# Kernel optimization log

Measured on AMD Instinct MI355X. Metric: run time of the kernel, lower is better.

Reference implementation:

```python
import jax, jax.numpy as jnp
import numpy as np

B, T, C, H = 2, 2048, 1024, 16  # batch, seq, d_model, heads
D = C // H                       # head dim = 64


def setup_inputs() -> dict:
    key = jax.random.key(0)
    ks = jax.random.split(key, 5)
    s = 0.02  # init scale for weights
    return {
        "x": jax.random.normal(ks[0], (B, T, C), jnp.float32),
        "Wq": jax.random.normal(ks[1], (C, C), jnp.float32) * s,
        "bq": jnp.zeros((C,), jnp.float32),
        "Wk": jax.random.normal(ks[2], (C, C), jnp.float32) * s,
        "bk": jnp.zeros((C,), jnp.float32),
        "Wv": jax.random.normal(ks[3], (C, C), jnp.float32) * s,
        "bv": jnp.zeros((C,), jnp.float32),
        "Wo": jax.random.normal(ks[4], (C, C), jnp.float32) * s,
        "bo": jnp.zeros((C,), jnp.float32),
    }


def reference(x, Wq, bq, Wk, bk, Wv, bv, Wo, bo):
    b, t, c = x.shape
    h, d = H, C // H
    # QKV projections (torch Linear: x @ W.T + b), split into heads: b h t d
    q = (x @ Wq.T + bq).reshape(b, t, h, d).transpose(0, 2, 1, 3)
    k = (x @ Wk.T + bk).reshape(b, t, h, d).transpose(0, 2, 1, 3)
    v = (x @ Wv.T + bv).reshape(b, t, h, d).transpose(0, 2, 1, 3)

    scale = 1.0 / float(np.sqrt(d))
    att = jnp.einsum("bhqd,bhkd->bhqk", q, k) * scale  # [B,H,T,T]
    causal = jnp.tril(jnp.ones((t, t), dtype=bool))
    att = jnp.where(causal[None, None, :, :], att, -jnp.inf)
    att = jax.nn.softmax(att, axis=-1)
    att_weights = att  # attn_dropout with p=0 is identity

    y = jnp.einsum("bhqk,bhkd->bhqd", att, v)          # [B,H,T,D]
    y = y.transpose(0, 2, 1, 3).reshape(b, t, c)        # b q (h d)
    y = y @ Wo.T + bo                                   # out proj; resid_dropout p=0
    return y, att_weights
```

## Files before the change

kernel.cpp:

```cpp
#include <hip/hip_runtime.h>

#define DI __device__ __forceinline__

typedef __attribute__((ext_vector_type(8))) short short8;
typedef __attribute__((ext_vector_type(4))) float floatx4;
typedef unsigned short u16;

#define Bb 2
#define Tt 2048
#define Cc 1024
#define Hh 16
#define Dd 64
#define C1 0.1803368801111244f
#define NEGBIG (-1e30f)

DI float bf2f(u16 u) { union { unsigned int i; float f; } v; v.i = ((unsigned int)u) << 16; return v.f; }
DI u16 f2bf(float f) {
  union { float f; unsigned int i; } v; v.f = f;
  unsigned int i = v.i;
  unsigned int r = i + 0x7fffu + ((i >> 16) & 1u);
  return (u16)(r >> 16);
}

DI floatx4 mfma16(short8 a, short8 b, floatx4 c) {
  return __builtin_amdgcn_mfma_f32_16x16x32_bf16(a, b, c, 0, 0, 0);
}

DI void gload16(const u16* g, u16* l) {
  __builtin_amdgcn_global_load_lds(
      (const __attribute__((address_space(1))) unsigned int*)(g),
      (__attribute__((address_space(3))) unsigned int*)(l), 16, 0, 0);
}

DI uint4 load8(const void* p, size_t eoff, int isbf) {
  if (isbf) {
    return *(const uint4*)((const u16*)p + eoff);
  } else {
    const float* f = (const float*)p + eoff;
    float4 a = *(const float4*)f;
    float4 b = *(const float4*)(f + 4);
    union { uint4 u; u16 s[8]; } r;
    r.s[0] = f2bf(a.x); r.s[1] = f2bf(a.y); r.s[2] = f2bf(a.z); r.s[3] = f2bf(a.w);
    r.s[4] = f2bf(b.x); r.s[5] = f2bf(b.y); r.s[6] = f2bf(b.z); r.s[7] = f2bf(b.w);
    return r.u;
  }
}

DI float loadb(const void* p, int i, int isbf) {
  return isbf ? bf2f(((const u16*)p)[i]) : ((const float*)p)[i];
}

__global__ void detect_dtype(const u16* __restrict__ x, int* __restrict__ flag) {
  __shared__ int cnt[256];
  int c = 0;
  for (int i = threadIdx.x; i < 4096; i += 256) {
    unsigned u = x[2 * i];
    unsigned e = (u >> 7) & 0xFFu;
    c += (e == 0u || (e >= 100u && e <= 150u)) ? 1 : 0;
  }
  cnt[threadIdx.x] = c;
  __syncthreads();
  for (int s = 128; s > 0; s >>= 1) {
    if ((int)threadIdx.x < s) cnt[threadIdx.x] += cnt[threadIdx.x + s];
    __syncthreads();
  }
  if (threadIdx.x == 0) *flag = (cnt[0] > 2458) ? 1 : 0;
}

__global__ __launch_bounds__(256) void convert_all(
    const void* __restrict__ x,
    const void* __restrict__ wq, const void* __restrict__ wk,
    const void* __restrict__ wv, const void* __restrict__ wo,
    u16* __restrict__ xb,
    u16* __restrict__ wqb, u16* __restrict__ wkb,
    u16* __restrict__ wvb, u16* __restrict__ wob,
    const int* __restrict__ flagp) {
  const int isbf = *flagp;
  const void* src;
  u16* dst;
  size_t n;
  switch (blockIdx.y) {
    case 0: src = x;  dst = xb;  n = (size_t)Bb * Tt * Cc; break;
    case 1: src = wq; dst = wqb; n = (size_t)Cc * Cc; break;
    case 2: src = wk; dst = wkb; n = (size_t)Cc * Cc; break;
    case 3: src = wv; dst = wvb; n = (size_t)Cc * Cc; break;
    default: src = wo; dst = wob; n = (size_t)Cc * Cc; break;
  }
  size_t i8 = ((size_t)blockIdx.x * 256 + threadIdx.x) * 8;
  size_t step = (size_t)gridDim.x * 256 * 8;
  for (; i8 < n; i8 += step) {
    uint4 v = load8(src, i8, isbf);
    *(uint4*)(dst + i8) = v;
  }
}

__global__ __launch_bounds__(256) void qkv_gemm(
    const u16* __restrict__ Xb,
    const u16* __restrict__ Wqb, const u16* __restrict__ Wkb, const u16* __restrict__ Wvb,
    const void* __restrict__ bq, const void* __restrict__ bk, const void* __restrict__ bv,
    u16* __restrict__ Qb, u16* __restrict__ Kb, u16* __restrict__ Vb,
    const int* __restrict__ flagp) {
  __shared__ __align__(16) u16 As[128 * 32];
  __shared__ __align__(16) u16 Bs[128 * 32];
  const int isbf = *flagp;
  const int z = blockIdx.z;
  const u16* W = (z == 0) ? Wqb : (z == 1) ? Wkb : Wvb;
  const void* bias = (z == 0) ? bq : (z == 1) ? bk : bv;
  u16* Out = (z == 0) ? Qb : (z == 1) ? Kb : Vb;

  const int m0 = blockIdx.y * 128, n0 = blockIdx.x * 128;
  const int tid = threadIdx.x;
  const int w = tid >> 6, lane = tid & 63, quad = lane >> 4, l15 = lane & 15;
  const int wm = w >> 1, wn = w & 1;

  floatx4 acc[4][4];
#pragma unroll
  for (int a = 0; a < 4; ++a)
#pragma unroll
    for (int b2 = 0; b2 < 4; ++b2) acc[a][b2] = (floatx4){0.f, 0.f, 0.f, 0.f};

  const int s0 = w * 128 + lane, s1 = s0 + 64;
  const int rA0 = s0 >> 2, c0 = (s0 & 3) * 8;
  const int rA1 = s1 >> 2, c1 = (s1 & 3) * 8;
  const u16* gA0 = Xb + (size_t)(m0 + rA0) * Cc + c0;
  const u16* gA1 = Xb + (size_t)(m0 + rA1) * Cc + c1;
  const u16* gB0 = W + (size_t)(n0 + rA0) * Cc + c0;
  const u16* gB1 = W + (size_t)(n0 + rA1) * Cc + c1;
  u16* lA0 = As + w * 1024;
  u16* lA1 = As + w * 1024 + 512;
  u16* lB0 = Bs + w * 1024;
  u16* lB1 = Bs + w * 1024 + 512;

  for (int k0 = 0; k0 < Cc; k0 += 32) {
    __syncthreads();
    gload16(gA0 + k0, lA0);
    gload16(gA1 + k0, lA1);
    gload16(gB0 + k0, lB0);
    gload16(gB1 + k0, lB1);
    __syncthreads();
    short8 af[4], bfv[4];
#pragma unroll
    for (int t = 0; t < 4; ++t)
      af[t] = *(const short8*)(As + (wm * 64 + t * 16 + l15) * 32 + quad * 8);
#pragma unroll
    for (int t = 0; t < 4; ++t)
      bfv[t] = *(const short8*)(Bs + (wn * 64 + t * 16 + l15) * 32 + quad * 8);
#pragma unroll
    for (int tm = 0; tm < 4; ++tm)
#pragma unroll
      for (int tn = 0; tn < 4; ++tn) acc[tm][tn] = mfma16(af[tm], bfv[tn], acc[tm][tn]);
  }

  float bb[4];
#pragma unroll
  for (int tn = 0; tn < 4; ++tn) bb[tn] = loadb(bias, n0 + wn * 64 + tn * 16 + l15, isbf);
#pragma unroll
  for (int tm = 0; tm < 4; ++tm) {
#pragma unroll
    for (int tn = 0; tn < 4; ++tn) {
      int n = n0 + wn * 64 + tn * 16 + l15;
      int h = n >> 6, d = n & 63;
#pragma unroll
      for (int r = 0; r < 4; ++r) {
        int m = m0 + wm * 64 + tm * 16 + quad * 4 + r;
        int b = m >> 11, t = m & 2047;
        Out[(((size_t)(b * Hh + h) * Tt) + t) * Dd + d] = f2bf(acc[tm][tn][r] + bb[tn]);
      }
    }
  }
}

__global__ __launch_bounds__(256) void out_gemm(
    const u16* __restrict__ Y, const u16* __restrict__ Wob, const void* __restrict__ bo,
    float* __restrict__ Out, const int* __restrict__ flagp) {
  __shared__ __align__(16) u16 As[128 * 32];
  __shared__ __align__(16) u16 Bs[128 * 32];
  const int isbf = *flagp;
  const int m0 = blockIdx.y * 128, n0 = blockIdx.x * 128;
  const int tid = threadIdx.x;
  const int w = tid >> 6, lane = tid & 63, quad = lane >> 4, l15 = lane & 15;
  const int wm = w >> 1, wn = w & 1;

  floatx4 acc[4][4];
#pragma unroll
  for (int a = 0; a < 4; ++a)
#pragma unroll
    for (int b2 = 0; b2 < 4; ++b2) acc[a][b2] = (floatx4){0.f, 0.f, 0.f, 0.f};

  const int s0 = w * 128 + lane, s1 = s0 + 64;
  const int rA0 = s0 >> 2, c0 = (s0 & 3) * 8;
  const int rA1 = s1 >> 2, c1 = (s1 & 3) * 8;
  const u16* gA0 = Y + (size_t)(m0 + rA0) * Cc + c0;
  const u16* gA1 = Y + (size_t)(m0 + rA1) * Cc + c1;
  const u16* gB0 = Wob + (size_t)(n0 + rA0) * Cc + c0;
  const u16* gB1 = Wob + (size_t)(n0 + rA1) * Cc + c1;
  u16* lA0 = As + w * 1024;
  u16* lA1 = As + w * 1024 + 512;
  u16* lB0 = Bs + w * 1024;
  u16* lB1 = Bs + w * 1024 + 512;

  for (int k0 = 0; k0 < Cc; k0 += 32) {
    __syncthreads();
    gload16(gA0 + k0, lA0);
    gload16(gA1 + k0, lA1);
    gload16(gB0 + k0, lB0);
    gload16(gB1 + k0, lB1);
    __syncthreads();
    short8 af[4], bfv[4];
#pragma unroll
    for (int t = 0; t < 4; ++t)
      af[t] = *(const short8*)(As + (wm * 64 + t * 16 + l15) * 32 + quad * 8);
#pragma unroll
    for (int t = 0; t < 4; ++t)
      bfv[t] = *(const short8*)(Bs + (wn * 64 + t * 16 + l15) * 32 + quad * 8);
#pragma unroll
    for (int tm = 0; tm < 4; ++tm)
#pragma unroll
      for (int tn = 0; tn < 4; ++tn) acc[tm][tn] = mfma16(af[tm], bfv[tn], acc[tm][tn]);
  }

  float bb[4];
#pragma unroll
  for (int tn = 0; tn < 4; ++tn) bb[tn] = loadb(bo, n0 + wn * 64 + tn * 16 + l15, isbf);
#pragma unroll
  for (int tm = 0; tm < 4; ++tm)
#pragma unroll
    for (int tn = 0; tn < 4; ++tn) {
      int n = n0 + wn * 64 + tn * 16 + l15;
#pragma unroll
      for (int r = 0; r < 4; ++r) {
        int m = m0 + wm * 64 + tm * 16 + quad * 4 + r;
        Out[(size_t)m * Cc + n] = acc[tm][tn][r] + bb[tn];
      }
    }
}

__global__ __launch_bounds__(256) void attn_kernel(
    const u16* __restrict__ Qbuf, const u16* __restrict__ Kbuf, const u16* __restrict__ Vbuf,
    float* __restrict__ Att, u16* __restrict__ Ybuf) {
  __shared__ __align__(16) u16 Qs[16 * 72];
  __shared__ __align__(16) u16 Ks[128 * 72];
  __shared__ __align__(16) u16 Vts[64 * 136];
  __shared__ __align__(16) u16 Ps[16 * 136];
  __shared__ float redM[4][16], redL[4][16];
  __shared__ float Mfin[16], Lfin[16];

  const int qt = blockIdx.x, h = blockIdx.y, b = blockIdx.z;
  const int q0 = qt * 16, q_hi = q0 + 15;
  const int tid = threadIdx.x;
  const int w = tid >> 6, lane = tid & 63, quad = lane >> 4, l15 = lane & 15;

  const size_t headoff = (size_t)(b * Hh + h) * Tt * Dd;
  const u16* Qh = Qbuf + headoff;
  const u16* Kh = Kbuf + headoff;
  const u16* Vh = Vbuf + headoff;
  float* attO = Att + (size_t)(b * Hh + h) * Tt * Tt;

  {
    int row = tid >> 4, c4 = tid & 15;
    *(uint2*)(Qs + row * 72 + c4 * 4) = *(const uint2*)(Qh + (size_t)(q0 + row) * Dd + c4 * 4);
  }
  __syncthreads();
  short8 aq0 = *(const short8*)(Qs + l15 * 72 + quad * 8);
  short8 aq1 = *(const short8*)(Qs + l15 * 72 + 32 + quad * 8);

  float m4[4], l4[4];
#pragma unroll
  for (int r = 0; r < 4; ++r) { m4[r] = NEGBIG; l4[r] = 0.f; }

  const int nact = (q_hi + 1 + 127) / 128;

  for (int c = 0; c < nact; ++c) {
    const int kb = c * 128;
    __syncthreads();
#pragma unroll
    for (int i = 0; i < 4; ++i) {
      int slot = tid + i * 256;
      int row = slot >> 3, c8 = slot & 7;
      *(uint4*)(Ks + row * 72 + c8 * 8) = *(const uint4*)(Kh + (size_t)(kb + row) * Dd + c8 * 8);
    }
    __syncthreads();
#pragma unroll
    for (int tile = 0; tile < 2; ++tile) {
      int kloc = w * 32 + tile * 16;
      floatx4 acc = (floatx4){0.f, 0.f, 0.f, 0.f};
      short8 b0 = *(const short8*)(Ks + (kloc + l15) * 72 + quad * 8);
      short8 b1 = *(const short8*)(Ks + (kloc + l15) * 72 + 32 + quad * 8);
      acc = mfma16(aq0, b0, acc);
      acc = mfma16(aq1, b1, acc);
      int key = kb + kloc + l15;
#pragma unroll
      for (int r = 0; r < 4; ++r) {
        int qi = q0 + quad * 4 + r;
        if (key <= qi) {
          float s2 = acc[r] * C1;
          float mo = m4[r];
          float mn = fmaxf(mo, s2);
          l4[r] = l4[r] * exp2f(mo - mn) + exp2f(s2 - mn);
          m4[r] = mn;
        }
      }
    }
  }

#pragma unroll
  for (int r = 0; r < 4; ++r) {
    float m = m4[r], l = l4[r];
#pragma unroll
    for (int off = 8; off >= 1; off >>= 1) {
      float mo = __shfl_xor(m, off, 64);
      float lo = __shfl_xor(l, off, 64);
      float mn = fmaxf(m, mo);
      l = l * exp2f(m - mn) + lo * exp2f(mo - mn);
      m = mn;
    }
    m4[r] = m; l4[r] = l;
  }
  if (l15 == 0) {
#pragma unroll
    for (int r = 0; r < 4; ++r) { redM[w][quad * 4 + r] = m4[r]; redL[w][quad * 4 + r] = l4[r]; }
  }
  __syncthreads();
  if (tid < 16) {
    float m = NEGBIG;
#pragma unroll
    for (int w2 = 0; w2 < 4; ++w2) m = fmaxf(m, redM[w2][tid]);
    float l = 0.f;
#pragma unroll
    for (int w2 = 0; w2 < 4; ++w2) l += redL[w2][tid] * exp2f(redM[w2][tid] - m);
    Mfin[tid] = m;
    Lfin[tid] = 1.0f / l;
  }
  __syncthreads();

  floatx4 yacc = (floatx4){0.f, 0.f, 0.f, 0.f};

  for (int c = 0; c < Tt / 128; ++c) {
    const int kb = c * 128;
    if (kb > q_hi) {
      uint4 z; z.x = 0u; z.y = 0u; z.z = 0u; z.w = 0u;
#pragma unroll
      for (int i = 0; i < 2; ++i) {
        int slot = tid + i * 256;
        int row = slot >> 5, g = slot & 31;
        *(uint4*)(attO + (size_t)(q0 + row) * Tt + kb + g * 4) = z;
      }
      continue;
    }
    __syncthreads();
#pragma unroll
    for (int i = 0; i < 4; ++i) {
      int slot = tid + i * 256;
      int row = slot >> 3, c8 = slot & 7;
      *(uint4*)(Ks + row * 72 + c8 * 8) = *(const uint4*)(Kh + (size_t)(kb + row) * Dd + c8 * 8);
    }
    {
      int row = tid >> 1, cb = (tid & 1) * 32;
      const u16* src = Vh + (size_t)(kb + row) * Dd + cb;
      union { uint4 u; u16 s[8]; } cv;
#pragma unroll
      for (int g = 0; g < 4; ++g) {
        cv.u = *(const uint4*)(src + g * 8);
#pragma unroll
        for (int j = 0; j < 8; ++j) Vts[(cb + g * 8 + j) * 136 + row] = cv.s[j];
      }
    }
    __syncthreads();

#pragma unroll
    for (int tile = 0; tile < 2; ++tile) {
      int kloc = w * 32 + tile * 16;
      floatx4 acc = (floatx4){0.f, 0.f, 0.f, 0.f};
      short8 b0 = *(const short8*)(Ks + (kloc + l15) * 72 + quad * 8);
      short8 b1 = *(const short8*)(Ks + (kloc + l15) * 72 + 32 + quad * 8);
      acc = mfma16(aq0, b0, acc);
      acc = mfma16(aq1, b1, acc);
      int key = kb + kloc + l15;
#pragma unroll
      for (int r = 0; r < 4; ++r) {
        int row = quad * 4 + r;
        int qi = q0 + row;
        float p = 0.f;
        if (key <= qi) p = exp2f(fminf(acc[r] * C1 - Mfin[row], 0.f)) * Lfin[row];
        attO[(size_t)qi * Tt + key] = p;
        Ps[row * 136 + kloc + l15] = f2bf(p);
      }
    }
    __syncthreads();

#pragma unroll
    for (int ks = 0; ks < 4; ++ks) {
      short8 ap = *(const short8*)(Ps + l15 * 136 + ks * 32 + quad * 8);
      short8 bv = *(const short8*)(Vts + (w * 16 + l15) * 136 + ks * 32 + quad * 8);
      yacc = mfma16(ap, bv, yacc);
    }
  }

#pragma unroll
  for (int r = 0; r < 4; ++r) {
    int qi = q0 + quad * 4 + r;
    Ybuf[(size_t)(b * Tt + qi) * Cc + h * Dd + w * 16 + l15] = f2bf(yacc[r]);
  }
}

extern "C" void kernel_launch(void* const* d_in, const int* in_sizes, int n_in,
                              void* d_out, int out_size, void* d_ws, size_t ws_size,
                              hipStream_t stream) {
  const void* x  = d_in[0];
  const void* Wq = d_in[1];
  const void* bq = d_in[2];
  const void* Wk = d_in[3];
  const void* bk = d_in[4];
  const void* Wv = d_in[5];
  const void* bv = d_in[6];
  const void* Wo = d_in[7];
  const void* bo = d_in[8];
  float* out = (float*)d_out;

  const size_t NTC = (size_t)Bb * Tt * Cc;
  const size_t CC = (size_t)Cc * Cc;

  char* wsb = (char*)d_ws;
  int* flag = (int*)wsb;
  u16* Qb = (u16*)(wsb + 256);
  u16* Kb = Qb + NTC;
  u16* Vb = Kb + NTC;
  u16* Yb = Vb + NTC;
  u16* Xb = Yb + NTC;
  u16* Wqb = Xb + NTC;
  u16* Wkb = Wqb + CC;
  u16* Wvb = Wkb + CC;
  u16* Wob = Wvb + CC;

  hipLaunchKernelGGL(detect_dtype, dim3(1), dim3(256), 0, stream, (const u16*)x, flag);
  hipLaunchKernelGGL(convert_all, dim3(512, 5), dim3(256), 0, stream,
                     x, Wq, Wk, Wv, Wo, Xb, Wqb, Wkb, Wvb, Wob, flag);
  hipLaunchKernelGGL(qkv_gemm, dim3(8, 32, 3), dim3(256), 0, stream,
                     Xb, Wqb, Wkb, Wvb, bq, bk, bv, Qb, Kb, Vb, flag);
  float* attOut = out + NTC;
  hipLaunchKernelGGL(attn_kernel, dim3(Tt / 16, Hh, Bb), dim3(256), 0, stream,
                     Qb, Kb, Vb, attOut, Yb);
  hipLaunchKernelGGL(out_gemm, dim3(8, 32, 1), dim3(256), 0, stream,
                     Yb, Wob, bo, out, flag);
}
```

Baseline: 796.3 us.

## Restructure attention into 128-row query tiles with causal load-balanced pairing

Each block now covers two 128-row query tiles of one head (tile zp and 15-zp), so every block does the same amount of causal work. Eight waves each own 16 query rows, and each K/V tile loaded into shared memory is reused across all 128 queries instead of 16. Softmax statistics are kept per wave with a blockwise max/sum over 128 keys, which removes the cross-wave reduction and extra syncs. Each wave computes all 64 output dims for its rows using a small per-wave P buffer. The trade-off is only 256 blocks of 512 threads and higher register pressure from the s[8] and yacc[4] arrays.

```diff
diff --git a/kernel.cpp b/kernel.cpp
--- a/kernel.cpp
+++ b/kernel.cpp
@@ -235,18 +235,18 @@
     }
 }
 
-__global__ __launch_bounds__(256) void attn_kernel(
+__global__ __launch_bounds__(512) void attn_kernel(
     const u16* __restrict__ Qbuf, const u16* __restrict__ Kbuf, const u16* __restrict__ Vbuf,
     float* __restrict__ Att, u16* __restrict__ Ybuf) {
-  __shared__ __align__(16) u16 Qs[16 * 72];
   __shared__ __align__(16) u16 Ks[128 * 72];
   __shared__ __align__(16) u16 Vts[64 * 136];
-  __shared__ __align__(16) u16 Ps[16 * 136];
-  __shared__ float redM[4][16], redL[4][16];
-  __shared__ float Mfin[16], Lfin[16];
-
-  const int qt = blockIdx.x, h = blockIdx.y, b = blockIdx.z;
-  const int q0 = qt * 16, q_hi = q0 + 15;
+  __shared__ __align__(16) u16 Ps[8 * 16 * 40];
+
+  const int id = blockIdx.x;
+  const int zp = id >> 5;
+  const int hb = id & 31;
+  const int b = hb >> 4, h = hb & 15;
+
   const int tid = threadIdx.x;
   const int w = tid >> 6, lane = tid & 63, quad = lane >> 4, l15 = lane & 15;
 
@@ -255,151 +255,156 @@
   const u16* Kh = Kbuf + headoff;
   const u16* Vh = Vbuf + headoff;
   float* attO = Att + (size_t)(b * Hh + h) * Tt * Tt;
-
-  {
-    int row = tid >> 4, c4 = tid & 15;
-    *(uint2*)(Qs + row * 72 + c4 * 4) = *(const uint2*)(Qh + (size_t)(q0 + row) * Dd + c4 * 4);
-  }
-  __syncthreads();
-  short8 aq0 = *(const short8*)(Qs + l15 * 72 + quad * 8);
-  short8 aq1 = *(const short8*)(Qs + l15 * 72 + 32 + quad * 8);
-
-  float m4[4], l4[4];
-#pragma unroll
-  for (int r = 0; r < 4; ++r) { m4[r] = NEGBIG; l4[r] = 0.f; }
-
-  const int nact = (q_hi + 1 + 127) / 128;
-
-  for (int c = 0; c < nact; ++c) {
-    const int kb = c * 128;
-    __syncthreads();
-#pragma unroll
-    for (int i = 0; i < 4; ++i) {
-      int slot = tid + i * 256;
-      int row = slot >> 3, c8 = slot & 7;
-      *(uint4*)(Ks + row * 72 + c8 * 8) = *(const uint4*)(Kh + (size_t)(kb + row) * Dd + c8 * 8);
+  u16* Psw = Ps + w * 640;
+
+  for (int half = 0; half < 2; ++half) {
+    const int qt = half ? (15 - zp) : zp;
+    const int q0 = qt * 128;
+    const int qw = q0 + w * 16;
+
+    short8 aq0 = *(const short8*)(Qh + (size_t)(qw + l15) * Dd + quad * 8);
+    short8 aq1 = *(const short8*)(Qh + (size_t)(qw + l15) * Dd + 32 + quad * 8);
+
+    float m4[4], l4[4];
+#pragma unroll
+    for (int r = 0; r < 4; ++r) { m4[r] = NEGBIG; l4[r] = 0.f; }
+
+    for (int c = 0; c <= qt; ++c) {
+      const int kb = c * 128;
+      __syncthreads();
+#pragma unroll
+      for (int i = 0; i < 2; ++i) {
+        int slot = tid + i * 512;
+        int rr = slot >> 3, g = slot & 7;
+        *(uint4*)(Ks + rr * 72 + g * 8) = *(const uint4*)(Kh + (size_t)(kb + rr) * Dd + g * 8);
+      }
+      __syncthreads();
+
+      floatx4 s[8];
+#pragma unroll
+      for (int kt = 0; kt < 8; ++kt) {
+        short8 b0 = *(const short8*)(Ks + (kt * 16 + l15) * 72 + quad * 8);
+        short8 b1 = *(const short8*)(Ks + (kt * 16 + l15) * 72 + 32 + quad * 8);
+        floatx4 t = (floatx4){0.f, 0.f, 0.f, 0.f};
+        t = mfma16(aq0, b0, t);
+        t = mfma16(aq1, b1, t);
+        s[kt] = t;
+      }
+
+      const bool partial = (kb + 127 > qw);
+#pragma unroll
+      for (int r = 0; r < 4; ++r) {
+        const int qi = qw + quad * 4 + r;
+        float e[8];
+        float bm = NEGBIG;
+#pragma unroll
+        for (int kt = 0; kt < 8; ++kt) {
+          float s2 = s[kt][r] * C1;
+          if (partial) {
+            int key = kb + kt * 16 + l15;
+            s2 = (key <= qi) ? s2 : NEGBIG;
+          }
+          e[kt] = s2;
+          bm = fmaxf(bm, s2);
+        }
+#pragma unroll
+        for (int off = 8; off >= 1; off >>= 1) bm = fmaxf(bm, __shfl_xor(bm, off, 64));
+        const float mn = fmaxf(m4[r], bm);
+        float sum = 0.f;
+#pragma unroll
+        for (int kt = 0; kt < 8; ++kt) sum += exp2f(e[kt] - mn);
+#pragma unroll
+        for (int off = 8; off >= 1; off >>= 1) sum += __shfl_xor(sum, off, 64);
+        l4[r] = l4[r] * exp2f(m4[r] - mn) + sum;
+        m4[r] = mn;
+      }
     }
-    __syncthreads();
-#pragma unroll
-    for (int tile = 0; tile < 2; ++tile) {
-      int kloc = w * 32 + tile * 16;
-      floatx4 acc = (floatx4){0.f, 0.f, 0.f, 0.f};
-      short8 b0 = *(const short8*)(Ks + (kloc + l15) * 72 + quad * 8);
-      short8 b1 = *(const short8*)(Ks + (kloc + l15) * 72 + 32 + quad * 8);
-      acc = mfma16(aq0, b0, acc);
-      acc = mfma16(aq1, b1, acc);
-      int key = kb + kloc + l15;
+
+    float lrec[4];
+#pragma unroll
+    for (int r = 0; r < 4; ++r) lrec[r] = 1.0f / l4[r];
+
+    floatx4 yacc[4];
+#pragma unroll
+    for (int dt = 0; dt < 4; ++dt) yacc[dt] = (floatx4){0.f, 0.f, 0.f, 0.f};
+
+    for (int c = 0; c < Tt / 128; ++c) {
+      const int kb = c * 128;
+      if (c > qt) {
+        uint4 z; z.x = 0u; z.y = 0u; z.z = 0u; z.w = 0u;
+#pragma unroll
+        for (int i = 0; i < 8; ++i) {
+          int slot = tid + i * 512;
+          int row = slot >> 5, g = slot & 31;
+          *(uint4*)(attO + (size_t)(q0 + row) * Tt + kb + g * 4) = z;
+        }
+        continue;
+      }
+      __syncthreads();
+#pragma unroll
+      for (int i = 0; i < 2; ++i) {
+        int slot = tid + i * 512;
+        int rr = slot >> 3, g = slot & 7;
+        *(uint4*)(Ks + rr * 72 + g * 8) = *(const uint4*)(Kh + (size_t)(kb + rr) * Dd + g * 8);
+      }
+      {
+        int vrow = tid >> 2, vcb = (tid & 3) * 16;
+        const u16* src = Vh + (size_t)(kb + vrow) * Dd + vcb;
+        union { uint4 u; u16 sv[8]; } cv;
+#pragma unroll
+        for (int g = 0; g < 2; ++g) {
+          cv.u = *(const uint4*)(src + g * 8);
+#pragma unroll
+          for (int j = 0; j < 8; ++j) Vts[(vcb + g * 8 + j) * 136 + vrow] = cv.sv[j];
+        }
+      }
+      __syncthreads();
+
+      floatx4 s[8];
+#pragma unroll
+      for (int kt = 0; kt < 8; ++kt) {
+        short8 b0 = *(const short8*)(Ks + (kt * 16 + l15) * 72 + quad * 8);
+        short8 b1 = *(const short8*)(Ks + (kt * 16 + l15) * 72 + 32 + quad * 8);
+        floatx4 t = (floatx4){0.f, 0.f, 0.f, 0.f};
+        t = mfma16(aq0, b0, t);
+        t = mfma16(aq1, b1, t);
+        s[kt] = t;
+      }
+
+      const bool partial = (kb + 127 > qw);
+#pragma unroll
+      for (int ks = 0; ks < 4; ++ks) {
+#pragma unroll
+        for (int kk = 0; kk < 2; ++kk) {
+          const int kt = ks * 2 + kk;
+#pragma unroll
+          for (int r = 0; r < 4; ++r) {
+            const int row = quad * 4 + r;
+            const int qi = qw + row;
+            const int key = kb + kt * 16 + l15;
+            float p = exp2f(s[kt][r] * C1 - m4[r]) * lrec[r];
+            if (partial && key > qi) p = 0.f;
+            attO[(size_t)qi * Tt + key] = p;
+            Psw[row * 40 + kk * 16 + l15] = f2bf(p);
+          }
+        }
+        short8 ap = *(const short8*)(Psw + l15 * 40 + quad * 8);
+#pragma unroll
+        for (int dt = 0; dt < 4; ++dt) {
+          short8 bv = *(const short8*)(Vts + (dt * 16 + l15) * 136 + ks * 32 + quad * 8);
+          yacc[dt] = mfma16(ap, bv, yacc[dt]);
+        }
+      }
+    }
+
+#pragma unroll
+    for (int dt = 0; dt < 4; ++dt) {
 #pragma unroll
       for (int r = 0; r < 4; ++r) {
-        int qi = q0 + quad * 4 + r;
-        if (key <= qi) {
-          float s2 = acc[r] * C1;
-          float mo = m4[r];
-          float mn = fmaxf(mo, s2);
-          l4[r] = l4[r] * exp2f(mo - mn) + exp2f(s2 - mn);
-          m4[r] = mn;
-        }
+        const int qi = qw + quad * 4 + r;
+        Ybuf[(size_t)(b * Tt + qi) * Cc + h * Dd + dt * 16 + l15] = f2bf(yacc[dt][r]);
       }
     }
-  }
-
-#pragma unroll
-  for (int r = 0; r < 4; ++r) {
-    float m = m4[r], l = l4[r];
-#pragma unroll
-    for (int off = 8; off >= 1; off >>= 1) {
-      float mo = __shfl_xor(m, off, 64);
-      float lo = __shfl_xor(l, off, 64);
-      float mn = fmaxf(m, mo);
-      l = l * exp2f(m - mn) + lo * exp2f(mo - mn);
-      m = mn;
-    }
-    m4[r] = m; l4[r] = l;
-  }
-  if (l15 == 0) {
-#pragma unroll
-    for (int r = 0; r < 4; ++r) { redM[w][quad * 4 + r] = m4[r]; redL[w][quad * 4 + r] = l4[r]; }
-  }
-  __syncthreads();
-  if (tid < 16) {
-    float m = NEGBIG;
-#pragma unroll
-    for (int w2 = 0; w2 < 4; ++w2) m = fmaxf(m, redM[w2][tid]);
-    float l = 0.f;
-#pragma unroll
-    for (int w2 = 0; w2 < 4; ++w2) l += redL[w2][tid] * exp2f(redM[w2][tid] - m);
-    Mfin[tid] = m;
-    Lfin[tid] = 1.0f / l;
-  }
-  __syncthreads();
-
-  floatx4 yacc = (floatx4){0.f, 0.f, 0.f, 0.f};
-
-  for (int c = 0; c < Tt / 128; ++c) {
-    const int kb = c * 128;
-    if (kb > q_hi) {
-      uint4 z; z.x = 0u; z.y = 0u; z.z = 0u; z.w = 0u;
-#pragma unroll
-      for (int i = 0; i < 2; ++i) {
-        int slot = tid + i * 256;
-        int row = slot >> 5, g = slot & 31;
-        *(uint4*)(attO + (size_t)(q0 + row) * Tt + kb + g * 4) = z;
-      }
-      continue;
-    }
-    __syncthreads();
-#pragma unroll
-    for (int i = 0; i < 4; ++i) {
-      int slot = tid + i * 256;
-      int row = slot >> 3, c8 = slot & 7;
-      *(uint4*)(Ks + row * 72 + c8 * 8) = *(const uint4*)(Kh + (size_t)(kb + row) * Dd + c8 * 8);
-    }
-    {
-      int row = tid >> 1, cb = (tid & 1) * 32;
-      const u16* src = Vh + (size_t)(kb + row) * Dd + cb;
-      union { uint4 u; u16 s[8]; } cv;
-#pragma unroll
-      for (int g = 0; g < 4; ++g) {
-        cv.u = *(const uint4*)(src + g * 8);
-#pragma unroll
-        for (int j = 0; j < 8; ++j) Vts[(cb + g * 8 + j) * 136 + row] = cv.s[j];
-      }
-    }
-    __syncthreads();
-
-#pragma unroll
-    for (int tile = 0; tile < 2; ++tile) {
-      int kloc = w * 32 + tile * 16;
-      floatx4 acc = (floatx4){0.f, 0.f, 0.f, 0.f};
-      short8 b0 = *(const short8*)(Ks + (kloc + l15) * 72 + quad * 8);
-      short8 b1 = *(const short8*)(Ks + (kloc + l15) * 72 + 32 + quad * 8);
-      acc = mfma16(aq0, b0, acc);
-      acc = mfma16(aq1, b1, acc);
-      int key = kb + kloc + l15;
-#pragma unroll
-      for (int r = 0; r < 4; ++r) {
-        int row = quad * 4 + r;
-        int qi = q0 + row;
-        float p = 0.f;
-        if (key <= qi) p = exp2f(fminf(acc[r] * C1 - Mfin[row], 0.f)) * Lfin[row];
-        attO[(size_t)qi * Tt + key] = p;
-        Ps[row * 136 + kloc + l15] = f2bf(p);
-      }
-    }
-    __syncthreads();
-
-#pragma unroll
-    for (int ks = 0; ks < 4; ++ks) {
-      short8 ap = *(const short8*)(Ps + l15 * 136 + ks * 32 + quad * 8);
-      short8 bv = *(const short8*)(Vts + (w * 16 + l15) * 136 + ks * 32 + quad * 8);
-      yacc = mfma16(ap, bv, yacc);
-    }
-  }
-
-#pragma unroll
-  for (int r = 0; r < 4; ++r) {
-    int qi = q0 + quad * 4 + r;
-    Ybuf[(size_t)(b * Tt + qi) * Cc + h * Dd + w * 16 + l15] = f2bf(yacc[r]);
   }
 }
 
@@ -438,7 +443,7 @@
   hipLaunchKernelGGL(qkv_gemm, dim3(8, 32, 3), dim3(256), 0, stream,
                      Xb, Wqb, Wkb, Wvb, bq, bk, bv, Qb, Kb, Vb, flag);
   float* attOut = out + NTC;
-  hipLaunchKernelGGL(attn_kernel, dim3(Tt / 16, Hh, Bb), dim3(256), 0, stream,
+  hipLaunchKernelGGL(attn_kernel, dim3(256), dim3(512), 0, stream,
                      Qb, Kb, Vb, attOut, Yb);
   hipLaunchKernelGGL(out_gemm, dim3(8, 32, 1), dim3(256), 0, stream,
                      Yb, Wob, bo, out, flag);
```

Result: faster. 709.7 us (-10.9%).
